# Performance work log

Measured on AMD Instinct MI355X. Metric: run time of the kernel, lower is better.

## Reference

```python
import jax, jax.numpy as jnp
import numpy as np

H = 16      # attention heads
D = 1024    # embedding size
HD = 64     # head size = D // H


def setup_inputs() -> dict:
    key = jax.random.key(0)
    ks = jax.random.split(key, 6)
    s = 1.0 / np.sqrt(D)
    x = jax.random.normal(ks[0], (2, 2048, D), dtype=jnp.float32)
    Wq = jax.random.normal(ks[1], (H, D, HD), dtype=jnp.float32) * s
    Wk = jax.random.normal(ks[2], (H, D, HD), dtype=jnp.float32) * s
    Wv = jax.random.normal(ks[3], (H, D, HD), dtype=jnp.float32) * s
    Wo = jax.random.normal(ks[4], (H * HD, D), dtype=jnp.float32) * s
    bo = jax.random.normal(ks[5], (D,), dtype=jnp.float32) * 0.01
    return {"x": x, "Wq": Wq, "Wk": Wk, "Wv": Wv, "Wo": Wo, "bo": bo}


def reference(x, Wq, Wk, Wv, Wo, bo):
    # x: [B, S, D]; per-head projections batched over the head axis.
    B, S, _ = x.shape
    q = jnp.einsum('bsd,hde->bhse', x, Wq)  # [B,H,S,HD]
    k = jnp.einsum('bsd,hde->bhse', x, Wk)
    v = jnp.einsum('bsd,hde->bhse', x, Wv)
    scale = 1.0 / jnp.sqrt(jnp.asarray(HD, dtype=x.dtype))
    scores = jnp.einsum('bhqe,bhke->bhqk', q, k) * scale  # [B,H,S,S]
    causal = jnp.tril(jnp.ones((S, S), dtype=bool))
    scores = jnp.where(causal, scores, jnp.asarray(-jnp.inf, dtype=x.dtype))
    attn = jax.nn.softmax(scores, axis=-1)
    out = jnp.einsum('bhqk,bhke->bhqe', attn, v)  # [B,H,S,HD]
    # concat heads along last dim (head order matches ModuleList order)
    out = out.transpose(0, 2, 1, 3).reshape(B, S, H * HD)
    return out @ Wo + bo  # dropout is identity in eval mode
```

## Files before the change

### kernel.cpp

```cpp
#include <hip/hip_runtime.h>
#include <hip/hip_bf16.h>
#include <cstdint>

#define Hh 16
#define Dd 1024
#define HD 64
#define Bb 2
#define Ss 2048

typedef float f32x4 __attribute__((ext_vector_type(4)));
typedef __bf16 bf16x8 __attribute__((ext_vector_type(8)));

__device__ __forceinline__ unsigned short f2bf(float f) {
  union { float f; unsigned u; } v; v.f = f;
  unsigned r = (v.u + 0x7FFFu + ((v.u >> 16) & 1u)) >> 16;
  return (unsigned short)r;
}

__device__ __forceinline__ void gld16(const void* g, void* l) {
  __builtin_amdgcn_global_load_lds(
      (__attribute__((address_space(1))) void*)(g),
      (__attribute__((address_space(3))) void*)(l),
      16, 0, 0);
}

__global__ __launch_bounds__(256)
void pack_x_k(const float4* __restrict__ x, unsigned short* __restrict__ xb, int n4) {
  const int i = blockIdx.x * blockDim.x + threadIdx.x;
  if (i >= n4) return;
  const float4 v = x[i];
  ushort4 o;
  o.x = f2bf(v.x); o.y = f2bf(v.y); o.z = f2bf(v.z); o.w = f2bf(v.w);
  *(ushort4*)&xb[(size_t)i * 4] = o;
}

__global__ __launch_bounds__(256)
void tconv_qkv(const float* __restrict__ Wq, const float* __restrict__ Wk,
               const float* __restrict__ Wv, unsigned short* __restrict__ out,
               float qscale) {
  __shared__ float T[64][65];
  const int m = blockIdx.z;
  const float* base = (m < 16) ? Wq : (m < 32) ? Wk : Wv;
  const float scale = (m < 16) ? qscale : 1.0f;
  const float* src = base + (size_t)(m & 15) * 1024 * 64;
  unsigned short* dst = out + (size_t)m * 1024 * 64;
  const int r0 = blockIdx.y * 64;
  const int tx = threadIdx.x & 63, ty = threadIdx.x >> 6;
#pragma unroll
  for (int it = 0; it < 16; ++it) {
    const int i = ty + it * 4;
    T[i][tx] = src[(size_t)(r0 + i) * 64 + tx];
  }
  __syncthreads();
#pragma unroll
  for (int it = 0; it < 16; ++it) {
    const int jj = ty + it * 4;
    dst[(size_t)jj * 1024 + r0 + tx] = f2bf(T[tx][jj] * scale);
  }
}

__global__ __launch_bounds__(256)
void tconv_k(const float* __restrict__ in, unsigned short* __restrict__ out,
             int R, int C) {
  __shared__ float T[64][65];
  const int c0 = blockIdx.x * 64, r0 = blockIdx.y * 64;
  const int tx = threadIdx.x & 63, ty = threadIdx.x >> 6;
#pragma unroll
  for (int it = 0; it < 16; ++it) {
    const int i = ty + it * 4;
    T[i][tx] = in[(size_t)(r0 + i) * C + c0 + tx];
  }
  __syncthreads();
#pragma unroll
  for (int it = 0; it < 16; ++it) {
    const int jj = ty + it * 4;
    out[(size_t)(c0 + jj) * R + r0 + tx] = f2bf(T[tx][jj]);
  }
}

__global__ __launch_bounds__(256)
void gemm_qkv(const unsigned short* __restrict__ A,
              const unsigned short* __restrict__ Bt,
              unsigned short* __restrict__ q_out,
              unsigned short* __restrict__ k_out,
              unsigned short* __restrict__ vt_out)
{
  __shared__ unsigned short As[128 * 64];
  __shared__ unsigned short Bs[128 * 64];

  const int K = 1024;
  const int tid = threadIdx.x;
  const int w = tid >> 6, lane = tid & 63;
  const int lo = lane & 15, hi = lane >> 4;
  const int wr = w >> 1, wc = w & 1;
  const int row0 = blockIdx.y * 128;
  const int col0 = blockIdx.x * 128;
  const bool isv = (col0 >= 2048);

  f32x4 acc[4][4] = {};

  const int srow = w * 32 + (lane >> 3);
  const int scol = ((lane & 7) ^ (lane >> 3)) * 8;
  const int swl  = (lo & 7) << 4;

  for (int t = 0; t < 16; ++t) {
    const int k0 = t * 64;
#pragma unroll
    for (int c = 0; c < 4; ++c) {
      const int rr = srow + c * 8;
      gld16(A  + (size_t)(row0 + rr) * K + (k0 + scol),
            (char*)As + (w * 4 + c) * 1024);
      gld16(Bt + (size_t)(col0 + rr) * K + (k0 + scol),
            (char*)Bs + (w * 4 + c) * 1024);
    }
    __syncthreads();
#pragma unroll
    for (int ks = 0; ks < 2; ++ks) {
      bf16x8 af[4], bfr[4];
#pragma unroll
      for (int i = 0; i < 4; ++i)
        af[i] = *(const bf16x8*)((const char*)As +
                 (wr * 64 + i * 16 + lo) * 128 + ((ks * 64 + hi * 16) ^ swl));
#pragma unroll
      for (int j = 0; j < 4; ++j)
        bfr[j] = *(const bf16x8*)((const char*)Bs +
                 (wc * 64 + j * 16 + lo) * 128 + ((ks * 64 + hi * 16) ^ swl));
      __builtin_amdgcn_s_setprio(1);
      if (isv) {
#pragma unroll
        for (int i = 0; i < 4; ++i)
#pragma unroll
          for (int j = 0; j < 4; ++j)
            acc[i][j] = __builtin_amdgcn_mfma_f32_16x16x32_bf16(af[i], bfr[j], acc[i][j], 0, 0, 0);
      } else {
#pragma unroll
        for (int i = 0; i < 4; ++i)
#pragma unroll
          for (int j = 0; j < 4; ++j)
            acc[i][j] = __builtin_amdgcn_mfma_f32_16x16x32_bf16(bfr[j], af[i], acc[i][j], 0, 0, 0);
      }
      __builtin_amdgcn_s_setprio(0);
    }
    __syncthreads();
  }

#pragma unroll
  for (int i = 0; i < 4; ++i) {
#pragma unroll
    for (int j = 0; j < 4; ++j) {
      if (isv) {
        const int grow = row0 + wr * 64 + i * 16 + hi * 4;
        const int gcol = col0 + wc * 64 + j * 16 + lo;
        const int hd = (gcol >> 6) & 15, e = gcol & 63;
        const int bb2 = grow >> 11, s = grow & 2047;
        ushort4 pk;
        pk.x = f2bf(acc[i][j][0]); pk.y = f2bf(acc[i][j][1]);
        pk.z = f2bf(acc[i][j][2]); pk.w = f2bf(acc[i][j][3]);
        *(ushort4*)&vt_out[((size_t)(bb2 * Hh + hd) * HD + e) * Ss + s] = pk;
      } else {
        const int m  = row0 + wr * 64 + i * 16 + lo;
        const int n0 = col0 + wc * 64 + j * 16 + hi * 4;
        const int p = n0 >> 10;
        const int hd = (n0 >> 6) & 15, e = n0 & 63;
        const int bb2 = m >> 11, s = m & 2047;
        unsigned short* dst = (p == 0) ? q_out : k_out;
        ushort4 pk;
        pk.x = f2bf(acc[i][j][0]); pk.y = f2bf(acc[i][j][1]);
        pk.z = f2bf(acc[i][j][2]); pk.w = f2bf(acc[i][j][3]);
        *(ushort4*)&dst[((size_t)(bb2 * Hh + hd) * Ss + s) * HD + e] = pk;
      }
    }
  }
}

__global__ __launch_bounds__(256)
void gemm_out(const unsigned short* __restrict__ A,
              const unsigned short* __restrict__ Bt,
              float* __restrict__ o_out,
              const float* __restrict__ bias)
{
  __shared__ unsigned short As[64 * 64];
  __shared__ unsigned short Bs[128 * 64];

  const int K = 1024, Ndim = 1024;
  const int tid = threadIdx.x;
  const int w = tid >> 6, lane = tid & 63;
  const int lo = lane & 15, hi = lane >> 4;
  const int wr = w >> 1, wc = w & 1;
  const int row0 = blockIdx.y * 64;
  const int col0 = blockIdx.x * 128;

  f32x4 acc[2][4] = {};

  const int sr   = lane >> 3;
  const int scol = ((lane & 7) ^ sr) * 8;
  const int swl  = (lo & 7) << 4;

  for (int t = 0; t < 16; ++t) {
    const int k0 = t * 64;
#pragma unroll
    for (int c = 0; c < 2; ++c)
      gld16(A + (size_t)(row0 + c * 32 + w * 8 + sr) * K + (k0 + scol),
            (char*)As + c * 4096 + w * 1024);
#pragma unroll
    for (int c = 0; c < 4; ++c)
      gld16(Bt + (size_t)(col0 + c * 32 + w * 8 + sr) * K + (k0 + scol),
            (char*)Bs + c * 4096 + w * 1024);
    __syncthreads();
#pragma unroll
    for (int ks = 0; ks < 2; ++ks) {
      bf16x8 af[2], bfr[4];
#pragma unroll
      for (int i = 0; i < 2; ++i)
        af[i] = *(const bf16x8*)((const char*)As +
                 (wr * 32 + i * 16 + lo) * 128 + ((ks * 64 + hi * 16) ^ swl));
#pragma unroll
      for (int j = 0; j < 4; ++j)
        bfr[j] = *(const bf16x8*)((const char*)Bs +
                 (wc * 64 + j * 16 + lo) * 128 + ((ks * 64 + hi * 16) ^ swl));
      __builtin_amdgcn_s_setprio(1);
#pragma unroll
      for (int i = 0; i < 2; ++i)
#pragma unroll
        for (int j = 0; j < 4; ++j)
          acc[i][j] = __builtin_amdgcn_mfma_f32_16x16x32_bf16(bfr[j], af[i], acc[i][j], 0, 0, 0);
      __builtin_amdgcn_s_setprio(0);
    }
    __syncthreads();
  }

#pragma unroll
  for (int i = 0; i < 2; ++i) {
#pragma unroll
    for (int j = 0; j < 4; ++j) {
      const int m  = row0 + wr * 32 + i * 16 + lo;
      const int n0 = col0 + wc * 64 + j * 16 + hi * 4;
      const float4 bv = *(const float4*)&bias[n0];
      float4 o;
      o.x = acc[i][j][0] + bv.x; o.y = acc[i][j][1] + bv.y;
      o.z = acc[i][j][2] + bv.z; o.w = acc[i][j][3] + bv.w;
      *(float4*)&o_out[(size_t)m * Ndim + n0] = o;
    }
  }
}

__global__ __launch_bounds__(256)
void attn_fwd(const unsigned short* __restrict__ qb,
              const unsigned short* __restrict__ kb,
              const unsigned short* __restrict__ vtb,
              unsigned short* __restrict__ ob)
{
  __shared__ unsigned short Ks[2][64 * 64];
  __shared__ unsigned short Vs[2][64 * 64];

  const int qt = 31 - blockIdx.y;
  const int bh = blockIdx.x;
  const int bb2 = bh >> 4;
  const int hd = bh & 15;

  const unsigned short* Q  = qb  + (size_t)bh * Ss * HD;
  const unsigned short* Kg = kb  + (size_t)bh * Ss * HD;
  const unsigned short* Vt = vtb + (size_t)bh * HD * Ss;

  const int tid = threadIdx.x;
  const int w = tid >> 6, lane = tid & 63;
  const int lo = lane & 15, hi = lane >> 4;
  const int qrow0 = qt * 64 + w * 16;

  const int sr   = lane >> 3;
  const int scol = ((lane & 7) ^ sr) * 8;
  int prow[2];
#pragma unroll
  for (int c = 0; c < 2; ++c) {
    const int L = c * 4 + w;
    prow[c] = (L >> 2) * 32 + ((L & 1) * 2 + (sr >> 2)) * 8 + ((L >> 1) & 1) * 4 + (sr & 3);
  }

#define STAGE(bi, kv)                                                     \
  _Pragma("unroll")                                                       \
  for (int c = 0; c < 2; ++c) {                                           \
    const int L = c * 4 + w;                                              \
    gld16(Kg + (size_t)((kv) + prow[c]) * HD + scol,                      \
          (char*)&Ks[bi][0] + L * 1024);                                  \
    gld16(Vt + (size_t)(L * 8 + sr) * Ss + (kv) + scol,                   \
          (char*)&Vs[bi][0] + L * 1024);                                  \
  }

  const int swl = (lo & 7) << 4;

  bf16x8 vones;
#pragma unroll
  for (int j = 0; j < 8; ++j) vones[j] = (__bf16)1.0f;

  bf16x8 qf[2];
#pragma unroll
  for (int ks = 0; ks < 2; ++ks)
    qf[ks] = *(const bf16x8*)&Q[(size_t)(qrow0 + lo) * HD + ks * 32 + hi * 8];

  f32x4 oacc[4] = {};
  float m2s = -INFINITY;
  float l2[4];
#pragma unroll
  for (int r = 0; r < 4; ++r) l2[r] = 0.f;

  const int ntiles = qt + 1;

  STAGE(0, 0);
  __syncthreads();

  int cur = 0;
  for (int t = 0; t < ntiles; ++t) {
    if (t + 1 < ntiles) { STAGE(cur ^ 1, (t + 1) * 64); }

    f32x4 sacc[4] = {};
    __builtin_amdgcn_s_setprio(1);
#pragma unroll
    for (int ks = 0; ks < 2; ++ks) {
      bf16x8 kf[4];
#pragma unroll
      for (int nj = 0; nj < 4; ++nj)
        kf[nj] = *(const bf16x8*)((const char*)&Ks[cur][0] +
                 (nj * 16 + lo) * 128 + ((ks * 64 + hi * 16) ^ swl));
#pragma unroll
      for (int nj = 0; nj < 4; ++nj)
        sacc[nj] = __builtin_amdgcn_mfma_f32_16x16x32_bf16(kf[nj], qf[ks], sacc[nj], 0, 0, 0);
    }
    __builtin_amdgcn_s_setprio(0);

    if (t == qt) {
      const int qr = w * 16 + lo;
#pragma unroll
      for (int nj = 0; nj < 4; ++nj) {
        const int kb0 = (nj >> 1) * 32 + (nj & 1) * 4 + hi * 8;
#pragma unroll
        for (int r = 0; r < 4; ++r)
          if (kb0 + r > qr) sacc[nj][r] = -INFINITY;
      }
    }

    float a0 = fmaxf(fmaxf(sacc[0][0], sacc[0][1]), fmaxf(sacc[0][2], sacc[0][3]));
    float a1 = fmaxf(fmaxf(sacc[1][0], sacc[1][1]), fmaxf(sacc[1][2], sacc[1][3]));
    float a2 = fmaxf(fmaxf(sacc[2][0], sacc[2][1]), fmaxf(sacc[2][2], sacc[2][3]));
    float a3 = fmaxf(fmaxf(sacc[3][0], sacc[3][1]), fmaxf(sacc[3][2], sacc[3][3]));
    const float lmax = fmaxf(fmaxf(a0, a1), fmaxf(a2, a3));
    if (!__all(lmax - m2s <= 8.0f)) {
      float rm = lmax;
      rm = fmaxf(rm, __shfl_xor(rm, 16, 64));
      rm = fmaxf(rm, __shfl_xor(rm, 32, 64));
      const float mn = fmaxf(m2s, rm);
      const float rcs = __builtin_amdgcn_exp2f(m2s - mn);
      m2s = mn;
#pragma unroll
      for (int r = 0; r < 4; ++r) {
        const float rc = __shfl(rcs, hi * 4 + r, 64);
        l2[r] *= rc;
#pragma unroll
        for (int nj = 0; nj < 4; ++nj)
          oacc[nj][r] *= rc;
      }
    }

    bf16x8 pa[2];
#pragma unroll
    for (int ks = 0; ks < 2; ++ks)
#pragma unroll
      for (int j = 0; j < 4; ++j) {
        pa[ks][j]     = (__bf16)__builtin_amdgcn_exp2f(sacc[2 * ks][j]     - m2s);
        pa[ks][4 + j] = (__bf16)__builtin_amdgcn_exp2f(sacc[2 * ks + 1][j] - m2s);
      }

    f32x4 osum = {};
    __builtin_amdgcn_s_setprio(1);
#pragma unroll
    for (int ks = 0; ks < 2; ++ks) {
      bf16x8 vf[4];
#pragma unroll
      for (int nj = 0; nj < 4; ++nj)
        vf[nj] = *(const bf16x8*)((const char*)&Vs[cur][0] +
                 (nj * 16 + lo) * 128 + ((ks * 64 + hi * 16) ^ swl));
#pragma unroll
      for (int nj = 0; nj < 4; ++nj)
        oacc[nj] = __builtin_amdgcn_mfma_f32_16x16x32_bf16(pa[ks], vf[nj], oacc[nj], 0, 0, 0);
      osum = __builtin_amdgcn_mfma_f32_16x16x32_bf16(pa[ks], vones, osum, 0, 0, 0);
    }
    __builtin_amdgcn_s_setprio(0);
#pragma unroll
    for (int r = 0; r < 4; ++r)
      l2[r] += osum[r];

    __syncthreads();
    cur ^= 1;
  }
#undef STAGE

#pragma unroll
  for (int r = 0; r < 4; ++r) {
    const int s = qrow0 + hi * 4 + r;
    const float il = 1.0f / l2[r];
    const size_t base = ((size_t)bb2 * Ss + s) * Dd + hd * HD;
#pragma unroll
    for (int nj = 0; nj < 4; ++nj)
      ob[base + nj * 16 + lo] = f2bf(oacc[nj][r] * il);
  }
}

extern "C" void kernel_launch(void* const* d_in, const int* in_sizes, int n_in,
                              void* d_out, int out_size, void* d_ws, size_t ws_size,
                              hipStream_t stream)
{
  const float* x  = (const float*)d_in[0];
  const float* Wq = (const float*)d_in[1];
  const float* Wk = (const float*)d_in[2];
  const float* Wv = (const float*)d_in[3];
  const float* Wo = (const float*)d_in[4];
  const float* bo = (const float*)d_in[5];
  float* out = (float*)d_out;

  char* ws = (char*)d_ws;
  unsigned short* xb    = (unsigned short*)(ws);
  unsigned short* wqkvT = (unsigned short*)(ws + 8388608);
  unsigned short* woT   = (unsigned short*)(ws + 14680064);
  unsigned short* qb    = (unsigned short*)(ws + 16777216);
  unsigned short* kb    = (unsigned short*)(ws + 25165824);
  unsigned short* vtb   = (unsigned short*)(ws + 33554432);
  unsigned short* ob    = (unsigned short*)(ws + 41943040);

  pack_x_k<<<4096, 256, 0, stream>>>((const float4*)x, xb, 1048576);
  tconv_qkv<<<dim3(1, 16, 48), 256, 0, stream>>>(Wq, Wk, Wv, wqkvT,
                                                 0.18033688011112042f);
  tconv_k<<<dim3(16, 16, 1), 256, 0, stream>>>(Wo, woT, 1024, 1024);

  gemm_qkv<<<dim3(24, 32), 256, 0, stream>>>(xb, wqkvT, qb, kb, vtb);
  attn_fwd<<<dim3(32, 32), 256, 0, stream>>>(qb, kb, vtb, ob);
  gemm_out<<<dim3(8, 64), 256, 0, stream>>>(ob, woT, out, bo);
}
```

Before: 124.4 us.

## Retile QKV GEMM to 256x256 blocks with double-buffered async LDS loads

The QKV projection GEMM moves from 128x128 tiles with 4 waves to 256x256 tiles with 8 waves. The K loop gets a two-stage LDS double buffer driven by explicit vmcnt waits and raw barriers, so global loads overlap with MFMA work. A block-index swizzle groups tiles for better L2 reuse. The cost is much larger LDS use (128KB per block) and more accumulator registers, and the grid shrinks to 192 blocks, which may not fill all CUs.

```diff
diff --git a/kernel.cpp b/kernel.cpp
--- a/kernel.cpp
+++ b/kernel.cpp
@@ -78,79 +78,97 @@
   }
 }
 
-__global__ __launch_bounds__(256)
+__global__ __launch_bounds__(512, 2)
 void gemm_qkv(const unsigned short* __restrict__ A,
               const unsigned short* __restrict__ Bt,
               unsigned short* __restrict__ q_out,
               unsigned short* __restrict__ k_out,
               unsigned short* __restrict__ vt_out)
 {
-  __shared__ unsigned short As[128 * 64];
-  __shared__ unsigned short Bs[128 * 64];
-
-  const int K = 1024;
+  __shared__ unsigned short As[2][256 * 64];
+  __shared__ unsigned short Bs[2][256 * 64];
+
+  const int K = 1024, NT = 16;
   const int tid = threadIdx.x;
   const int w = tid >> 6, lane = tid & 63;
   const int lo = lane & 15, hi = lane >> 4;
-  const int wr = w >> 1, wc = w & 1;
-  const int row0 = blockIdx.y * 128;
-  const int col0 = blockIdx.x * 128;
+  const int wm = w >> 2, wn = w & 3;
+
+  const int bid = blockIdx.x;
+  const int swz = (bid & 7) * 24 + (bid >> 3);
+  const int col0 = (swz % 12) * 256;
+  const int row0 = (swz / 12) * 256;
   const bool isv = (col0 >= 2048);
 
-  f32x4 acc[4][4] = {};
-
-  const int srow = w * 32 + (lane >> 3);
-  const int scol = ((lane & 7) ^ (lane >> 3)) * 8;
-  const int swl  = (lo & 7) << 4;
-
-  for (int t = 0; t < 16; ++t) {
-    const int k0 = t * 64;
-#pragma unroll
-    for (int c = 0; c < 4; ++c) {
-      const int rr = srow + c * 8;
-      gld16(A  + (size_t)(row0 + rr) * K + (k0 + scol),
-            (char*)As + (w * 4 + c) * 1024);
-      gld16(Bt + (size_t)(col0 + rr) * K + (k0 + scol),
-            (char*)Bs + (w * 4 + c) * 1024);
-    }
-    __syncthreads();
+  f32x4 acc[8][4] = {};
+
+  const int srow = tid >> 3;
+  const int scol = ((tid & 7) ^ (srow & 7)) * 8;
+  const int ldso = (w << 3) * 128;
+
+#define QSTAGE(bi, k0)                                                   \
+  _Pragma("unroll")                                                      \
+  for (int cc = 0; cc < 4; ++cc) {                                       \
+    gld16(A  + (size_t)(row0 + cc * 64 + srow) * K + ((k0) + scol),      \
+          (char*)&As[bi][0] + cc * 8192 + ldso);                         \
+    gld16(Bt + (size_t)(col0 + cc * 64 + srow) * K + ((k0) + scol),      \
+          (char*)&Bs[bi][0] + cc * 8192 + ldso);                         \
+  }
+
+  const int swl = (lo & 7) << 4;
+
+  QSTAGE(0, 0);
+  QSTAGE(1, 64);
+  asm volatile("s_waitcnt vmcnt(8)" ::: "memory");
+  asm volatile("s_barrier" ::: "memory");
+
+  for (int t = 0; t < NT; ++t) {
+    const int c = t & 1;
+    const char* Apt = (const char*)&As[c][0] + (wm * 128) * 128;
+    const char* Bpt = (const char*)&Bs[c][0] + (wn * 64) * 128;
 #pragma unroll
     for (int ks = 0; ks < 2; ++ks) {
-      bf16x8 af[4], bfr[4];
-#pragma unroll
-      for (int i = 0; i < 4; ++i)
-        af[i] = *(const bf16x8*)((const char*)As +
-                 (wr * 64 + i * 16 + lo) * 128 + ((ks * 64 + hi * 16) ^ swl));
+      bf16x8 af[8], bfr[4];
+#pragma unroll
+      for (int i = 0; i < 8; ++i)
+        af[i] = *(const bf16x8*)(Apt + (i * 16 + lo) * 128 + ((ks * 64 + hi * 16) ^ swl));
 #pragma unroll
       for (int j = 0; j < 4; ++j)
-        bfr[j] = *(const bf16x8*)((const char*)Bs +
-                 (wc * 64 + j * 16 + lo) * 128 + ((ks * 64 + hi * 16) ^ swl));
+        bfr[j] = *(const bf16x8*)(Bpt + (j * 16 + lo) * 128 + ((ks * 64 + hi * 16) ^ swl));
       __builtin_amdgcn_s_setprio(1);
       if (isv) {
 #pragma unroll
-        for (int i = 0; i < 4; ++i)
+        for (int i = 0; i < 8; ++i)
 #pragma unroll
           for (int j = 0; j < 4; ++j)
             acc[i][j] = __builtin_amdgcn_mfma_f32_16x16x32_bf16(af[i], bfr[j], acc[i][j], 0, 0, 0);
       } else {
 #pragma unroll
-        for (int i = 0; i < 4; ++i)
+        for (int i = 0; i < 8; ++i)
 #pragma unroll
           for (int j = 0; j < 4; ++j)
             acc[i][j] = __builtin_amdgcn_mfma_f32_16x16x32_bf16(bfr[j], af[i], acc[i][j], 0, 0, 0);
       }
       __builtin_amdgcn_s_setprio(0);
     }
-    __syncthreads();
-  }
-
-#pragma unroll
-  for (int i = 0; i < 4; ++i) {
+    asm volatile("s_barrier" ::: "memory");
+    if (t + 2 < NT) {
+      QSTAGE(c, (t + 2) * 64);
+      asm volatile("s_waitcnt vmcnt(8)" ::: "memory");
+    } else if (t + 1 < NT) {
+      asm volatile("s_waitcnt vmcnt(0)" ::: "memory");
+    }
+    asm volatile("s_barrier" ::: "memory");
+  }
+#undef QSTAGE
+
+#pragma unroll
+  for (int i = 0; i < 8; ++i) {
 #pragma unroll
     for (int j = 0; j < 4; ++j) {
       if (isv) {
-        const int grow = row0 + wr * 64 + i * 16 + hi * 4;
-        const int gcol = col0 + wc * 64 + j * 16 + lo;
+        const int grow = row0 + wm * 128 + i * 16 + hi * 4;
+        const int gcol = col0 + wn * 64 + j * 16 + lo;
         const int hd = (gcol >> 6) & 15, e = gcol & 63;
         const int bb2 = grow >> 11, s = grow & 2047;
         ushort4 pk;
@@ -158,8 +176,8 @@
         pk.z = f2bf(acc[i][j][2]); pk.w = f2bf(acc[i][j][3]);
         *(ushort4*)&vt_out[((size_t)(bb2 * Hh + hd) * HD + e) * Ss + s] = pk;
       } else {
-        const int m  = row0 + wr * 64 + i * 16 + lo;
-        const int n0 = col0 + wc * 64 + j * 16 + hi * 4;
+        const int m  = row0 + wm * 128 + i * 16 + lo;
+        const int n0 = col0 + wn * 64 + j * 16 + hi * 4;
         const int p = n0 >> 10;
         const int hd = (n0 >> 6) & 15, e = n0 & 63;
         const int bb2 = m >> 11, s = m & 2047;
@@ -430,7 +448,7 @@
                                                  0.18033688011112042f);
   tconv_k<<<dim3(16, 16, 1), 256, 0, stream>>>(Wo, woT, 1024, 1024);
 
-  gemm_qkv<<<dim3(24, 32), 256, 0, stream>>>(xb, wqkvT, qb, kb, vtb);
+  gemm_qkv<<<dim3(192), 512, 0, stream>>>(xb, wqkvT, qb, kb, vtb);
   attn_fwd<<<dim3(32, 32), 256, 0, stream>>>(qb, kb, vtb, ob);
   gemm_out<<<dim3(8, 64), 256, 0, stream>>>(ob, woT, out, bo);
 }
```

New measurement: 262.9 us. 111% more time.
